# Performance work log

Measured on AMD Instinct MI355X. Metric: run time of the kernel, lower is better.

Reference implementation:

```python
import jax, jax.numpy as jnp
import numpy as np

NUM_GROUPS = 32
EPS = 1e-5


def group_norm(x, gamma, beta):
    # x: [B, C, H, W]; normalize per group of C//NUM_GROUPS channels over (c_in_group, H, W)
    B, C, H, W = x.shape
    xg = x.reshape(B, NUM_GROUPS, C // NUM_GROUPS, H, W)
    mean = jnp.mean(xg, axis=(2, 3, 4), keepdims=True)
    var = jnp.var(xg, axis=(2, 3, 4), keepdims=True)
    xn = ((xg - mean) * jax.lax.rsqrt(var + EPS)).reshape(B, C, H, W)
    return xn * gamma[None, :, None, None] + beta[None, :, None, None]


def setup_inputs() -> dict:
    key = jax.random.key(0)
    kx, kq, kp = jax.random.split(key, 3)
    B, C, H, W = 4, 256, 64, 64
    x = jax.random.normal(kx, (B, C, H, W), dtype=jnp.float32)
    gamma = jnp.ones((C,), dtype=jnp.float32)
    beta = jnp.zeros((C,), dtype=jnp.float32)
    # 1x1 convs == channel matmuls; weights [out_c, in_c]
    w_qkv = jax.random.normal(kq, (3 * C, C), dtype=jnp.float32) / np.sqrt(C)
    w_proj = jax.random.normal(kp, (C, C), dtype=jnp.float32) / np.sqrt(C)
    return {"x": x, "t": 0, "gamma": gamma, "beta": beta, "w_qkv": w_qkv, "w_proj": w_proj}


def reference(x, t, gamma, beta, w_qkv, w_proj):
    B, C, H, W = x.shape
    normed = group_norm(x, gamma, beta)  # [B,C,H,W]
    qkv = jnp.einsum('bchw,oc->bohw', normed, w_qkv)  # [B,3C,H,W]
    q, k, v = jnp.split(qkv, 3, axis=1)
    N = H * W
    q = q.reshape(B, C, N)
    k = k.reshape(B, C, N)
    v = v.reshape(B, C, N)
    # scores[b,i,j] = sum_c q[b,c,i] k[b,c,j] / sqrt(C)
    scores = jnp.einsum('bci,bcj->bij', q, k) / jnp.sqrt(jnp.asarray(C, x.dtype))
    attn = jax.nn.softmax(scores, axis=-1)  # [B,N,N]
    # out[b,c,i] = sum_j v[b,c,j] attn[b,i,j]
    out = jnp.einsum('bcj,bij->bci', v, attn).reshape(B, C, H, W)
    out = jnp.einsum('bchw,oc->bohw', out, w_proj)
    return x + out
```

## Files before the change

kernel.cpp:

```cpp
#include <hip/hip_runtime.h>

typedef __bf16 bf16x8 __attribute__((ext_vector_type(8)));
typedef float floatx4 __attribute__((ext_vector_type(4)));
typedef float floatx16 __attribute__((ext_vector_type(16)));
typedef unsigned int u32;

#define BB 4
#define CC 256
#define NN 4096

__device__ __forceinline__ unsigned short f2bf(float f) {
  union { float f; unsigned u; } v; v.f = f;
  unsigned r = v.u + 0x7fffu + ((v.u >> 16) & 1u);
  return (unsigned short)(r >> 16);
}

__device__ __forceinline__ float bf2f(unsigned short s) {
  union { unsigned u; float f; } v; v.u = ((u32)s) << 16;
  return v.f;
}

__device__ __forceinline__ void async16(const void* g, void* l) {
  __builtin_amdgcn_global_load_lds((const __attribute__((address_space(1))) u32*)g,
                                   (__attribute__((address_space(3))) u32*)l, 16, 0, 0);
}

__device__ __forceinline__ u32 fbits(float f) {
  union { float f; u32 u; } v; v.f = f; return v.u;
}

__global__ __launch_bounds__(256) void gn_stats_wconv(const float* __restrict__ x, float* __restrict__ mr,
                                                      const float* __restrict__ wqkv, const float* __restrict__ wproj,
                                                      unsigned short* __restrict__ wq_bf, unsigned short* __restrict__ wp_bf) {
  if (blockIdx.x < 1024) {
    int i = blockIdx.x * 256 + threadIdx.x;
    if (i < 196608) {
      float v = wqkv[i];
      if (i < 65536) v *= 0.090168440055560213f;
      wq_bf[i] = f2bf(v);
    } else {
      int j = i - 196608;
      wp_bf[j] = f2bf(wproj[j]);
    }
    return;
  }
  int bg = blockIdx.x - 1024;
  const float* p = x + (size_t)bg * 32768;
  int t = threadIdx.x;
  float s = 0.f, q = 0.f;
#pragma unroll
  for (int it = 0; it < 32; ++it) {
    float4 v = *(const float4*)(p + it * 1024 + t * 4);
    s += v.x + v.y + v.z + v.w;
    q += v.x * v.x + v.y * v.y + v.z * v.z + v.w * v.w;
  }
#pragma unroll
  for (int off = 1; off < 64; off <<= 1) {
    s += __shfl_xor(s, off, 64);
    q += __shfl_xor(q, off, 64);
  }
  __shared__ float red[8];
  int w = t >> 6;
  if ((t & 63) == 0) { red[w] = s; red[4 + w] = q; }
  __syncthreads();
  if (t == 0) {
    float S = red[0] + red[1] + red[2] + red[3];
    float Q = red[4] + red[5] + red[6] + red[7];
    float mean = S * (1.f / 32768.f);
    float var = Q * (1.f / 32768.f) - mean * mean;
    mr[bg] = mean;
    mr[128 + bg] = rsqrtf(var + 1e-5f);
  }
}

__global__ __launch_bounds__(256) void gn_apply(const float* __restrict__ x, const float* __restrict__ mr,
                                                const float* __restrict__ gamma, const float* __restrict__ beta,
                                                unsigned short* __restrict__ normed) {
  int bid = blockIdx.x;
  int nt = bid & 63;
  int ct = (bid >> 6) & 3;
  int b = bid >> 8;
  int c0 = ct * 64, n0 = nt * 64;
  __shared__ unsigned short T[64][80];
  int t = threadIdx.x;
#pragma unroll
  for (int it = 0; it < 4; ++it) {
    int idx = it * 256 + t;
    int cl = idx >> 4;
    int n4 = (idx & 15) * 4;
    int c = c0 + cl;
    int bg = b * 32 + (c >> 3);
    float mean = mr[bg], rstd = mr[128 + bg];
    float sc = rstd * gamma[c];
    float sh = beta[c] - mean * sc;
    float4 v = *(const float4*)(x + ((size_t)(b * CC + c)) * NN + n0 + n4);
    T[n4 + 0][cl] = f2bf(v.x * sc + sh);
    T[n4 + 1][cl] = f2bf(v.y * sc + sh);
    T[n4 + 2][cl] = f2bf(v.z * sc + sh);
    T[n4 + 3][cl] = f2bf(v.w * sc + sh);
  }
  __syncthreads();
#pragma unroll
  for (int it = 0; it < 2; ++it) {
    int idx = it * 256 + t;
    int nl = idx >> 3, ck = idx & 7;
    uint4 val;
    unsigned short* pv = (unsigned short*)&val;
#pragma unroll
    for (int j = 0; j < 8; ++j) pv[j] = T[nl][ck * 8 + j];
    *(uint4*)(normed + ((size_t)b * NN + n0 + nl) * CC + c0 + ck * 8) = val;
  }
}

template <int RESID>
__global__ __launch_bounds__(256, 2) void gemm_bt2(const unsigned short* __restrict__ A,
                                                   const unsigned short* __restrict__ Bm,
                                                   void* __restrict__ Cout, const float* __restrict__ resid,
                                                   int mtiles, int ldc,
                                                   long sA, long sB, long sC, long sR) {
  __shared__ __attribute__((aligned(16))) char smem[65536];
  int mt = blockIdx.x % mtiles;
  int nt = blockIdx.x / mtiles;
  int b = blockIdx.y;
  int m0 = mt * 128, n0 = nt * 128;
  int t = threadIdx.x, w = t >> 6, l = t & 63;
  int l16 = l & 15, quad = l >> 4;
  int wr = w >> 1, wc = w & 1;
  const unsigned short* Ab = A + (size_t)b * sA + (size_t)m0 * 256;
  const unsigned short* Bb = Bm + (size_t)b * sB + (size_t)n0 * 256;

  auto stage = [&](int kb, int buf) {
    int rsub = l >> 3;
    int cj = (l & 7) ^ rsub;
    char* ab = smem + buf * 16384;
    char* bb = smem + 32768 + buf * 16384;
#pragma unroll
    for (int it = 0; it < 4; ++it) {
      int pp = w * 4 + it;
      size_t go = (size_t)(8 * pp + rsub) * 256 + kb * 64 + cj * 8;
      async16(Ab + go, ab + pp * 1024);
      async16(Bb + go, bb + pp * 1024);
    }
  };

  floatx4 acc[4][4];
#pragma unroll
  for (int m = 0; m < 4; ++m)
#pragma unroll
    for (int n = 0; n < 4; ++n)
#pragma unroll
      for (int r = 0; r < 4; ++r) acc[m][n][r] = 0.f;

  stage(0, 0);

#pragma unroll 1
  for (int kb = 0; kb < 4; ++kb) {
    int cur = kb & 1;
    __syncthreads();
    if (kb < 3) stage(kb + 1, cur ^ 1);
    const unsigned short* As = (const unsigned short*)(smem + cur * 16384);
    const unsigned short* Bs = (const unsigned short*)(smem + 32768 + cur * 16384);
#pragma unroll
    for (int kk = 0; kk < 2; ++kk) {
      bf16x8 af[4], bfr[4];
      int sw = ((kk * 4 + quad) ^ (l16 & 7)) * 8;
#pragma unroll
      for (int m = 0; m < 4; ++m)
        af[m] = *(const bf16x8*)&As[(wr * 64 + m * 16 + l16) * 64 + sw];
#pragma unroll
      for (int n = 0; n < 4; ++n)
        bfr[n] = *(const bf16x8*)&Bs[(wc * 64 + n * 16 + l16) * 64 + sw];
#pragma unroll
      for (int m = 0; m < 4; ++m)
#pragma unroll
        for (int n = 0; n < 4; ++n)
          acc[m][n] = __builtin_amdgcn_mfma_f32_16x16x32_bf16(af[m], bfr[n], acc[m][n], 0, 0, 0);
    }
  }

  size_t cb = (size_t)b * sC;
  size_t rb = (size_t)b * sR;
#pragma unroll
  for (int m = 0; m < 4; ++m)
#pragma unroll
    for (int n = 0; n < 4; ++n)
#pragma unroll
      for (int r = 0; r < 4; ++r) {
        int row = m0 + wr * 64 + m * 16 + quad * 4 + r;
        int col = n0 + wc * 64 + n * 16 + l16;
        size_t idx = (size_t)row * ldc + col;
        if (RESID)
          ((float*)Cout)[cb + idx] = acc[m][n][r] + resid[rb + idx];
        else
          ((unsigned short*)Cout)[cb + idx] = f2bf(acc[m][n][r]);
      }
}

__global__ __launch_bounds__(512, 2) void attn(const unsigned short* __restrict__ qk,
                                               const unsigned short* __restrict__ vbuf,
                                               unsigned short* __restrict__ opart0,
                                               unsigned short* __restrict__ opart1,
                                               float* __restrict__ lpart) {
  __shared__ __attribute__((aligned(16))) char smem[131072];

  int xcd = blockIdx.x & 7, slot = blockIdx.x >> 3;
  int b = xcd >> 1;
  int kh = xcd & 1;
  int i0 = slot * 128;
  int k0 = kh * 32;

  int t = threadIdx.x, w = t >> 6, l = t & 63;
  int l31 = l & 31, hi = l >> 5;
  int jh = w & 1;
  int iq = w >> 1;

  const size_t bqk = (size_t)b * NN * 512;
  const size_t bv = (size_t)b * CC * NN;

  auto stage = [&](int tile, int buf) {
    const unsigned short* kg = qk + bqk + (size_t)tile * 64 * 512 + 256;
    char* kb = smem + buf * 32768;
#pragma unroll
    for (int it = 0; it < 4; ++it) {
      int pp = w * 4 + it;
      int r = 2 * pp + (l >> 5);
      int c = (l & 31) ^ (r & 31);
      async16(kg + (size_t)r * 512 + c * 8, kb + pp * 1024);
    }
    const unsigned short* vg = vbuf + bv + (size_t)tile * 64;
    char* vb = smem + 65536 + buf * 32768;
    int cj = (l & 7) ^ ((l >> 3) & 7);
#pragma unroll
    for (int it = 0; it < 4; ++it) {
      int pp = w * 4 + it;
      int rc = 8 * pp + (l >> 3);
      async16(vg + (size_t)rc * NN + cj * 8, vb + pp * 1024);
    }
  };

  stage(k0, 0);

  bf16x8 qreg[16];
  {
    const unsigned short* qp = qk + bqk + (size_t)(i0 + iq * 32 + l31) * 512 + hi * 8;
#pragma unroll
    for (int ks = 0; ks < 16; ++ks)
      qreg[ks] = *(const bf16x8*)(qp + ks * 16);
  }

  floatx16 oacc[8];
#pragma unroll
  for (int cf = 0; cf < 8; ++cf)
#pragma unroll
    for (int r = 0; r < 16; ++r) oacc[cf][r] = 0.f;
  float lacc = 0.f;

  for (int kt = 0; kt < 32; ++kt) {
    int cur = kt & 1;
    __syncthreads();
    if (kt < 31) stage(k0 + kt + 1, cur ^ 1);

    const unsigned short* Kc = (const unsigned short*)(smem + cur * 32768);
    const unsigned short* Vc = (const unsigned short*)(smem + 65536 + cur * 32768);

    floatx16 st;
#pragma unroll
    for (int r = 0; r < 16; ++r) st[r] = 0.f;
#pragma unroll
    for (int ks = 0; ks < 16; ++ks) {
      bf16x8 kf = *(const bf16x8*)&Kc[(jh * 32 + l31) * 256 + (((ks << 1) | hi) ^ l31) * 8];
      st = __builtin_amdgcn_mfma_f32_32x32x16_bf16(kf, qreg[ks], st, 0, 0, 0);
    }

    u32 pr[8];
#pragma unroll
    for (int k2 = 0; k2 < 8; ++k2) {
      float p0 = __builtin_amdgcn_exp2f(st[2 * k2]);
      float p1 = __builtin_amdgcn_exp2f(st[2 * k2 + 1]);
      lacc += p0 + p1;
      pr[k2] = __builtin_amdgcn_perm(fbits(p1), fbits(p0), 0x07060302u);
    }

    union U { u32 u[4]; bf16x8 v; } a0, a1;
    {
      u32 sA = hi ? pr[0] : pr[2], sB = hi ? pr[1] : pr[3];
      u32 rA = (u32)__shfl_xor((int)sA, 32, 64);
      u32 rB = (u32)__shfl_xor((int)sB, 32, 64);
      a0.u[0] = hi ? rA : pr[0]; a0.u[1] = hi ? rB : pr[1];
      a0.u[2] = hi ? pr[2] : rA; a0.u[3] = hi ? pr[3] : rB;
      sA = hi ? pr[4] : pr[6]; sB = hi ? pr[5] : pr[7];
      rA = (u32)__shfl_xor((int)sA, 32, 64);
      rB = (u32)__shfl_xor((int)sB, 32, 64);
      a1.u[0] = hi ? rA : pr[4]; a1.u[1] = hi ? rB : pr[5];
      a1.u[2] = hi ? pr[6] : rA; a1.u[3] = hi ? pr[7] : rB;
    }

#pragma unroll
    for (int cf = 0; cf < 8; ++cf) {
      const unsigned short* vrow = Vc + (cf * 32 + l31) * 64;
      bf16x8 v0 = *(const bf16x8*)(vrow + (((jh * 4) | hi) ^ (l31 & 7)) * 8);
      oacc[cf] = __builtin_amdgcn_mfma_f32_32x32x16_bf16(a0.v, v0, oacc[cf], 0, 0, 0);
      bf16x8 v1 = *(const bf16x8*)(vrow + (((jh * 4 + 2) | hi) ^ (l31 & 7)) * 8);
      oacc[cf] = __builtin_amdgcn_mfma_f32_32x32x16_bf16(a1.v, v1, oacc[cf], 0, 0, 0);
    }
  }

  float l2 = lacc + __shfl_xor(lacc, 32, 64);

  float* Of = (float*)smem + iq * 8192;
  __syncthreads();
  if (jh == 1) {
#pragma unroll
    for (int cf = 0; cf < 8; ++cf)
#pragma unroll
      for (int r = 0; r < 16; ++r) {
        int il = (r & 3) + 8 * (r >> 2) + 4 * hi;
        Of[il * 256 + cf * 32 + l31] = oacc[cf][r];
      }
  }
  __syncthreads();
  unsigned short* ops = kh ? opart1 : opart0;
  size_t rowbase = (size_t)b * NN + i0 + iq * 32;
  if (jh == 0) {
#pragma unroll
    for (int cf = 0; cf < 8; ++cf)
#pragma unroll
      for (int r = 0; r < 16; ++r) {
        int il = (r & 3) + 8 * (r >> 2) + 4 * hi;
        float v = oacc[cf][r] + Of[il * 256 + cf * 32 + l31];
        ops[(rowbase + il) * CC + cf * 32 + l31] = f2bf(v);
      }
  }
  __syncthreads();
  float* Lred = (float*)smem;
  if (hi == 0) Lred[w * 32 + l31] = l2;
  __syncthreads();
  if (jh == 0 && hi == 0) {
    size_t pbl = (size_t)(b * 2 + kh) * NN + i0;
    lpart[pbl + iq * 32 + l31] = Lred[(iq * 2) * 32 + l31] + Lred[(iq * 2 + 1) * 32 + l31];
  }
}

__global__ __launch_bounds__(256) void gemm_proj(const unsigned short* __restrict__ wp,
                                                 const unsigned short* __restrict__ op0,
                                                 const unsigned short* __restrict__ op1,
                                                 const float* __restrict__ lp,
                                                 float* __restrict__ out, const float* __restrict__ x) {
  int mt = blockIdx.x & 1;
  int nt = blockIdx.x >> 1;
  int b = blockIdx.y;
  int m0 = mt * 128, n0 = nt * 128;
  __shared__ unsigned short As[128][72];
  __shared__ unsigned short Bs[128][72];
  __shared__ float Linv[128];
  int t = threadIdx.x;
  int w = t >> 6, lane = t & 63;
  int l16 = lane & 15, quad = lane >> 4;
  int wr = w >> 1, wc = w & 1;
  const unsigned short* Ab = wp + (size_t)m0 * 256;
  const unsigned short* o0 = op0 + ((size_t)b * NN + n0) * 256;
  const unsigned short* o1 = op1 + ((size_t)b * NN + n0) * 256;
  if (t < 128) Linv[t] = 1.f / (lp[b * 8192 + n0 + t] + lp[b * 8192 + 4096 + n0 + t]);
  floatx4 acc[4][4];
#pragma unroll
  for (int m = 0; m < 4; ++m)
#pragma unroll
    for (int n = 0; n < 4; ++n)
#pragma unroll
      for (int r = 0; r < 4; ++r) acc[m][n][r] = 0.f;

  for (int kb = 0; kb < 4; ++kb) {
    __syncthreads();
#pragma unroll
    for (int i = 0; i < 4; ++i) {
      int idx = i * 256 + t;
      int r = idx >> 3, ck = idx & 7;
      *(uint4*)&As[r][ck * 8] = *(const uint4*)(Ab + (size_t)r * 256 + kb * 64 + ck * 8);
      uint4 u0 = *(const uint4*)(o0 + (size_t)r * 256 + kb * 64 + ck * 8);
      uint4 u1 = *(const uint4*)(o1 + (size_t)r * 256 + kb * 64 + ck * 8);
      float li = Linv[r];
      const unsigned short* pa = (const unsigned short*)&u0;
      const unsigned short* pb = (const unsigned short*)&u1;
      union { unsigned short us[8]; uint4 q; } ob;
#pragma unroll
      for (int j = 0; j < 8; ++j)
        ob.us[j] = f2bf((bf2f(pa[j]) + bf2f(pb[j])) * li);
      *(uint4*)&Bs[r][ck * 8] = ob.q;
    }
    __syncthreads();
#pragma unroll
    for (int kk = 0; kk < 2; ++kk) {
      bf16x8 af[4], bfr[4];
#pragma unroll
      for (int m = 0; m < 4; ++m) af[m] = *(const bf16x8*)&As[wr * 64 + m * 16 + l16][kk * 32 + quad * 8];
#pragma unroll
      for (int n = 0; n < 4; ++n) bfr[n] = *(const bf16x8*)&Bs[wc * 64 + n * 16 + l16][kk * 32 + quad * 8];
#pragma unroll
      for (int m = 0; m < 4; ++m)
#pragma unroll
        for (int n = 0; n < 4; ++n)
          acc[m][n] = __builtin_amdgcn_mfma_f32_16x16x32_bf16(af[m], bfr[n], acc[m][n], 0, 0, 0);
    }
  }
  size_t cb = (size_t)b * CC * NN;
#pragma unroll
  for (int m = 0; m < 4; ++m)
#pragma unroll
    for (int n = 0; n < 4; ++n)
#pragma unroll
      for (int r = 0; r < 4; ++r) {
        int row = m0 + wr * 64 + m * 16 + quad * 4 + r;
        int col = n0 + wc * 64 + n * 16 + l16;
        size_t idx = cb + (size_t)row * NN + col;
        out[idx] = acc[m][n][r] + x[idx];
      }
}

extern "C" void kernel_launch(void* const* d_in, const int* in_sizes, int n_in,
                              void* d_out, int out_size, void* d_ws, size_t ws_size,
                              hipStream_t stream) {
  const float* x     = (const float*)d_in[0];
  const float* gamma = (const float*)d_in[2];
  const float* beta  = (const float*)d_in[3];
  const float* wqkv  = (const float*)d_in[4];
  const float* wproj = (const float*)d_in[5];
  float* out = (float*)d_out;

  char* p = (char*)d_ws;
  float* mr               = (float*)(p + 0);
  unsigned short* wq_bf   = (unsigned short*)(p + 1024);
  unsigned short* wp_bf   = (unsigned short*)(p + 394240);
  unsigned short* normed  = (unsigned short*)(p + 525312);
  unsigned short* qkbuf   = (unsigned short*)(p + 8913920);
  unsigned short* vbuf    = (unsigned short*)(p + 25691136);
  unsigned short* opart1  = (unsigned short*)(p + 34079744);
  unsigned short* opart0  = normed;
  float* lpart            = (float*)(p + 1024);
  unsigned short* wv_bf   = wq_bf + 512 * 256;

  gn_stats_wconv<<<1152, 256, 0, stream>>>(x, mr, wqkv, wproj, wq_bf, wp_bf);
  gn_apply<<<1024, 256, 0, stream>>>(x, mr, gamma, beta, normed);
  gemm_bt2<0><<<dim3(128, 4), 256, 0, stream>>>(normed, wq_bf, qkbuf, nullptr,
                                                32, 512, (long)NN * CC, 0L, (long)NN * 512, 0L);
  gemm_bt2<0><<<dim3(64, 4), 256, 0, stream>>>(wv_bf, normed, vbuf, nullptr,
                                               2, 4096, 0L, (long)NN * CC, (long)CC * NN, 0L);
  attn<<<256, 512, 0, stream>>>(qkbuf, vbuf, opart0, opart1, lpart);
  gemm_proj<<<dim3(64, 4), 256, 0, stream>>>(wp_bf, opart0, opart1, lpart, out, x);
}
```

Measured before the change: 195.4 us.

## Merge QK and V GEMM launches; pipeline projection GEMM with async loads

Combines the QK and V projection GEMMs into one launch that picks its operands from the block index, removing one kernel launch and the tail between them. The output-projection GEMM is rewritten with smaller 128x64 tiles and twice as many blocks. It double-buffers A through async global-to-LDS loads with a swizzled layout and prefetches the next B tile into registers during compute. This targets better occupancy and overlap in the final GEMM, at the cost of more LDS per block and more complex staging.

```diff
diff --git a/kernel.cpp b/kernel.cpp
--- a/kernel.cpp
+++ b/kernel.cpp
@@ -112,22 +112,35 @@
   }
 }
 
-template <int RESID>
-__global__ __launch_bounds__(256, 2) void gemm_bt2(const unsigned short* __restrict__ A,
-                                                   const unsigned short* __restrict__ Bm,
-                                                   void* __restrict__ Cout, const float* __restrict__ resid,
-                                                   int mtiles, int ldc,
-                                                   long sA, long sB, long sC, long sR) {
+__global__ __launch_bounds__(256, 2) void gemm_qkv_v(const unsigned short* __restrict__ normed,
+                                                     const unsigned short* __restrict__ wq_bf,
+                                                     const unsigned short* __restrict__ wv_bf,
+                                                     unsigned short* __restrict__ qkbuf,
+                                                     unsigned short* __restrict__ vbuf) {
   __shared__ __attribute__((aligned(16))) char smem[65536];
-  int mt = blockIdx.x % mtiles;
-  int nt = blockIdx.x / mtiles;
   int b = blockIdx.y;
-  int m0 = mt * 128, n0 = nt * 128;
+  const unsigned short *Ab, *Bb;
+  unsigned short* Cb;
+  int ldc, m0, n0;
+  if (blockIdx.x < 128) {
+    int mt = blockIdx.x % 32, nt = blockIdx.x / 32;
+    m0 = mt * 128; n0 = nt * 128;
+    Ab = normed + (size_t)b * NN * CC + (size_t)m0 * 256;
+    Bb = wq_bf + (size_t)n0 * 256;
+    Cb = qkbuf + (size_t)b * NN * 512;
+    ldc = 512;
+  } else {
+    int xx = blockIdx.x - 128;
+    int mt = xx & 1, nt = xx >> 1;
+    m0 = mt * 128; n0 = nt * 128;
+    Ab = wv_bf + (size_t)m0 * 256;
+    Bb = normed + (size_t)b * NN * CC + (size_t)n0 * 256;
+    Cb = vbuf + (size_t)b * CC * NN;
+    ldc = NN;
+  }
   int t = threadIdx.x, w = t >> 6, l = t & 63;
   int l16 = l & 15, quad = l >> 4;
   int wr = w >> 1, wc = w & 1;
-  const unsigned short* Ab = A + (size_t)b * sA + (size_t)m0 * 256;
-  const unsigned short* Bb = Bm + (size_t)b * sB + (size_t)n0 * 256;
 
   auto stage = [&](int kb, int buf) {
     int rsub = l >> 3;
@@ -178,8 +191,6 @@
     }
   }
 
-  size_t cb = (size_t)b * sC;
-  size_t rb = (size_t)b * sR;
 #pragma unroll
   for (int m = 0; m < 4; ++m)
 #pragma unroll
@@ -188,11 +199,7 @@
       for (int r = 0; r < 4; ++r) {
         int row = m0 + wr * 64 + m * 16 + quad * 4 + r;
         int col = n0 + wc * 64 + n * 16 + l16;
-        size_t idx = (size_t)row * ldc + col;
-        if (RESID)
-          ((float*)Cout)[cb + idx] = acc[m][n][r] + resid[rb + idx];
-        else
-          ((unsigned short*)Cout)[cb + idx] = f2bf(acc[m][n][r]);
+        Cb[(size_t)row * ldc + col] = f2bf(acc[m][n][r]);
       }
 }
 
@@ -341,76 +348,109 @@
   }
 }
 
-__global__ __launch_bounds__(256) void gemm_proj(const unsigned short* __restrict__ wp,
-                                                 const unsigned short* __restrict__ op0,
-                                                 const unsigned short* __restrict__ op1,
-                                                 const float* __restrict__ lp,
-                                                 float* __restrict__ out, const float* __restrict__ x) {
+__global__ __launch_bounds__(256, 2) void gemm_proj(const unsigned short* __restrict__ wp,
+                                                    const unsigned short* __restrict__ op0,
+                                                    const unsigned short* __restrict__ op1,
+                                                    const float* __restrict__ lp,
+                                                    float* __restrict__ out, const float* __restrict__ x) {
+  __shared__ __attribute__((aligned(16))) char smem[51456];
   int mt = blockIdx.x & 1;
   int nt = blockIdx.x >> 1;
   int b = blockIdx.y;
-  int m0 = mt * 128, n0 = nt * 128;
-  __shared__ unsigned short As[128][72];
-  __shared__ unsigned short Bs[128][72];
-  __shared__ float Linv[128];
-  int t = threadIdx.x;
-  int w = t >> 6, lane = t & 63;
-  int l16 = lane & 15, quad = lane >> 4;
+  int m0 = mt * 128, n0 = nt * 64;
+  int t = threadIdx.x, w = t >> 6, l = t & 63;
+  int l16 = l & 15, quad = l >> 4;
   int wr = w >> 1, wc = w & 1;
   const unsigned short* Ab = wp + (size_t)m0 * 256;
-  const unsigned short* o0 = op0 + ((size_t)b * NN + n0) * 256;
-  const unsigned short* o1 = op1 + ((size_t)b * NN + n0) * 256;
-  if (t < 128) Linv[t] = 1.f / (lp[b * 8192 + n0 + t] + lp[b * 8192 + 4096 + n0 + t]);
-  floatx4 acc[4][4];
+  float* Linv = (float*)(smem + 51200);
+
+  auto stageA = [&](int kb, int buf) {
+    int rsub = l >> 3;
+    int cj = (l & 7) ^ rsub;
+    char* ab = smem + buf * 16384;
+#pragma unroll
+    for (int it = 0; it < 4; ++it) {
+      int pp = w * 4 + it;
+      size_t go = (size_t)(8 * pp + rsub) * 256 + kb * 64 + cj * 8;
+      async16(Ab + go, ab + pp * 1024);
+    }
+  };
+
+  int brow = t >> 2;
+  int bck = (t & 3) * 16;
+  size_t bgo_base = ((size_t)b * NN + n0 + brow) * 256 + bck;
+  uint4 b0a, b0b, b1a, b1b;
+  auto loadB = [&](int kb) {
+    size_t go = bgo_base + kb * 64;
+    b0a = *(const uint4*)(op0 + go);
+    b0b = *(const uint4*)(op0 + go + 8);
+    b1a = *(const uint4*)(op1 + go);
+    b1b = *(const uint4*)(op1 + go + 8);
+  };
+
+  if (t < 64) Linv[t] = 1.f / (lp[b * 8192 + n0 + t] + lp[b * 8192 + 4096 + n0 + t]);
+  stageA(0, 0);
+  loadB(0);
+  __syncthreads();
+
+  floatx4 acc[4][2];
 #pragma unroll
   for (int m = 0; m < 4; ++m)
 #pragma unroll
-    for (int n = 0; n < 4; ++n)
+    for (int n = 0; n < 2; ++n)
 #pragma unroll
       for (int r = 0; r < 4; ++r) acc[m][n][r] = 0.f;
 
+#pragma unroll 1
   for (int kb = 0; kb < 4; ++kb) {
+    int cur = kb & 1;
+    {
+      float li = Linv[brow];
+      unsigned short* Bs = (unsigned short*)(smem + 32768 + cur * 9216);
+      const unsigned short* pa = (const unsigned short*)&b0a;
+      const unsigned short* pc = (const unsigned short*)&b1a;
+      union { unsigned short us[8]; uint4 q; } o1_, o2_;
+#pragma unroll
+      for (int j = 0; j < 8; ++j) o1_.us[j] = f2bf((bf2f(pa[j]) + bf2f(pc[j])) * li);
+      pa = (const unsigned short*)&b0b;
+      pc = (const unsigned short*)&b1b;
+#pragma unroll
+      for (int j = 0; j < 8; ++j) o2_.us[j] = f2bf((bf2f(pa[j]) + bf2f(pc[j])) * li);
+      *(uint4*)&Bs[brow * 72 + bck] = o1_.q;
+      *(uint4*)&Bs[brow * 72 + bck + 8] = o2_.q;
+    }
+    if (kb < 3) loadB(kb + 1);
     __syncthreads();
-#pragma unroll
-    for (int i = 0; i < 4; ++i) {
-      int idx = i * 256 + t;
-      int r = idx >> 3, ck = idx & 7;
-      *(uint4*)&As[r][ck * 8] = *(const uint4*)(Ab + (size_t)r * 256 + kb * 64 + ck * 8);
-      uint4 u0 = *(const uint4*)(o0 + (size_t)r * 256 + kb * 64 + ck * 8);
-      uint4 u1 = *(const uint4*)(o1 + (size_t)r * 256 + kb * 64 + ck * 8);
-      float li = Linv[r];
-      const unsigned short* pa = (const unsigned short*)&u0;
-      const unsigned short* pb = (const unsigned short*)&u1;
-      union { unsigned short us[8]; uint4 q; } ob;
-#pragma unroll
-      for (int j = 0; j < 8; ++j)
-        ob.us[j] = f2bf((bf2f(pa[j]) + bf2f(pb[j])) * li);
-      *(uint4*)&Bs[r][ck * 8] = ob.q;
-    }
-    __syncthreads();
+    if (kb < 3) stageA(kb + 1, cur ^ 1);
+    const unsigned short* As = (const unsigned short*)(smem + cur * 16384);
+    const unsigned short* Bs = (const unsigned short*)(smem + 32768 + cur * 9216);
 #pragma unroll
     for (int kk = 0; kk < 2; ++kk) {
-      bf16x8 af[4], bfr[4];
-#pragma unroll
-      for (int m = 0; m < 4; ++m) af[m] = *(const bf16x8*)&As[wr * 64 + m * 16 + l16][kk * 32 + quad * 8];
-#pragma unroll
-      for (int n = 0; n < 4; ++n) bfr[n] = *(const bf16x8*)&Bs[wc * 64 + n * 16 + l16][kk * 32 + quad * 8];
+      bf16x8 af[4], bfr[2];
+      int sw = ((kk * 4 + quad) ^ (l16 & 7)) * 8;
 #pragma unroll
       for (int m = 0; m < 4; ++m)
-#pragma unroll
-        for (int n = 0; n < 4; ++n)
+        af[m] = *(const bf16x8*)&As[(wr * 64 + m * 16 + l16) * 64 + sw];
+#pragma unroll
+      for (int n = 0; n < 2; ++n)
+        bfr[n] = *(const bf16x8*)&Bs[(wc * 32 + n * 16 + l16) * 72 + kk * 32 + quad * 8];
+#pragma unroll
+      for (int m = 0; m < 4; ++m)
+#pragma unroll
+        for (int n = 0; n < 2; ++n)
           acc[m][n] = __builtin_amdgcn_mfma_f32_16x16x32_bf16(af[m], bfr[n], acc[m][n], 0, 0, 0);
     }
   }
+
   size_t cb = (size_t)b * CC * NN;
 #pragma unroll
   for (int m = 0; m < 4; ++m)
 #pragma unroll
-    for (int n = 0; n < 4; ++n)
+    for (int n = 0; n < 2; ++n)
 #pragma unroll
       for (int r = 0; r < 4; ++r) {
         int row = m0 + wr * 64 + m * 16 + quad * 4 + r;
-        int col = n0 + wc * 64 + n * 16 + l16;
+        int col = n0 + wc * 32 + n * 16 + l16;
         size_t idx = cb + (size_t)row * NN + col;
         out[idx] = acc[m][n][r] + x[idx];
       }
@@ -440,10 +480,7 @@
 
   gn_stats_wconv<<<1152, 256, 0, stream>>>(x, mr, wqkv, wproj, wq_bf, wp_bf);
   gn_apply<<<1024, 256, 0, stream>>>(x, mr, gamma, beta, normed);
-  gemm_bt2<0><<<dim3(128, 4), 256, 0, stream>>>(normed, wq_bf, qkbuf, nullptr,
-                                                32, 512, (long)NN * CC, 0L, (long)NN * 512, 0L);
-  gemm_bt2<0><<<dim3(64, 4), 256, 0, stream>>>(wv_bf, normed, vbuf, nullptr,
-                                               2, 4096, 0L, (long)NN * CC, (long)CC * NN, 0L);
+  gemm_qkv_v<<<dim3(192, 4), 256, 0, stream>>>(normed, wq_bf, wv_bf, qkbuf, vbuf);
   attn<<<256, 512, 0, stream>>>(qkbuf, vbuf, opart0, opart1, lpart);
-  gemm_proj<<<dim3(64, 4), 256, 0, stream>>>(wp_bf, opart0, opart1, lpart, out, x);
-}
+  gemm_proj<<<dim3(128, 4), 256, 0, stream>>>(wp_bf, opart0, opart1, lpart, out, x);
+}
```

Result: faster. 187.9 us (median of 2 runs) (-3.9%).
